# Optimization experiments

Hardware: AMD Instinct MI355X
Metric: run time of the kernel (lower is better)

## Reference

```python
import jax, jax.numpy as jnp
import numpy as np

HEAD_SIZE = 64
SCALE = HEAD_SIZE ** -0.5


def setup_inputs() -> dict:
    key = jax.random.key(0)
    ks = jax.random.split(key, 7)
    B, T, E, H = 32, 2048, 1024, HEAD_SIZE
    x = jax.random.normal(ks[0], (B, T, E), dtype=jnp.float32)
    Wq = jax.random.normal(ks[1], (E, H), dtype=jnp.float32) * (E ** -0.5)
    bq = jax.random.normal(ks[2], (H,), dtype=jnp.float32) * 0.02
    Wk = jax.random.normal(ks[3], (E, H), dtype=jnp.float32) * (E ** -0.5)
    bk = jax.random.normal(ks[4], (H,), dtype=jnp.float32) * 0.02
    Wv = jax.random.normal(ks[5], (E, H), dtype=jnp.float32) * (E ** -0.5)
    bv = jax.random.normal(ks[6], (H,), dtype=jnp.float32) * 0.02
    return {"x": x, "Wq": Wq, "bq": bq, "Wk": Wk, "bk": bk, "Wv": Wv, "bv": bv}


def reference(x, Wq, bq, Wk, bk, Wv, bv):
    # Faithful to the torch source: the tril buffer is all ones so the mask is a
    # no-op, and F.softmax's result is discarded. Output = (Q K^T * scale) @ V.
    Q = x @ Wq + bq          # [B, T, H]
    K = x @ Wk + bk          # [B, T, H]
    V = x @ Wv + bv          # [B, T, H]
    wei = jnp.einsum('bqh,bkh->bqk', Q, K) * SCALE  # [B, T, T]
    return jnp.einsum('bqk,bkh->bqh', wei, V)       # [B, T, H]
```

## Files before the change

kernel.cpp:

```cpp
#include <hip/hip_runtime.h>
#include <hip/hip_bf16.h>


using bf16x8 = __attribute__((ext_vector_type(8))) short;
using f32x4  = __attribute__((ext_vector_type(4))) float;
using u32x4  = __attribute__((ext_vector_type(4))) unsigned int;
using u32x2  = __attribute__((ext_vector_type(2))) unsigned int;
using u16    = unsigned short;

__device__ __forceinline__ u16 f2bf(float f) {
    unsigned u = __builtin_bit_cast(unsigned, f);
    u += 0x7fffu + ((u >> 16) & 1u);
    return (u16)(u >> 16);
}

__global__ __launch_bounds__(256) void k_wt(const float* __restrict__ Wq,
                                            const float* __restrict__ Wk,
                                            const float* __restrict__ Wv,
                                            u16* __restrict__ WT) {
    __shared__ float Wl[64][68];
    const int seg = blockIdx.x >> 4, chunk = blockIdx.x & 15;
    const float* W = (seg == 0) ? Wq : (seg == 1) ? Wk : Wv;
    const int e0 = chunk * 64;
    const int tid = threadIdx.x;
    const int lr = tid >> 4, lc = (tid & 15) * 4;
#pragma unroll
    for (int p = 0; p < 4; ++p)
        *(f32x4*)&Wl[lr + p * 16][lc] = *(const f32x4*)(W + (size_t)(e0 + lr + p * 16) * 64 + lc);
    __syncthreads();
    const int c = tid >> 2, eb = (tid & 3) * 16;
    u16* const dst = WT + (size_t)(seg * 64 + c) * 1024 + e0;
#pragma unroll
    for (int q = 0; q < 16; ++q) {
        const int w = eb + q;
        const int kap = ((w >> 5) << 5) | (((w >> 2) & 3) << 3) |
                        (((w >> 4) & 1) << 2) | (w & 3);
        dst[kap] = f2bf(Wl[w][c]);
    }
}

__global__ __launch_bounds__(256, 3) void k_qkv(const float* __restrict__ x,
                                                const u16* __restrict__ WT,
                                                const float* __restrict__ bq,
                                                const float* __restrict__ bk,
                                                const float* __restrict__ bv,
                                                u16* __restrict__ Qb,
                                                float* __restrict__ part) {
    __shared__ __align__(16) char lds[49152];
    const int tid  = threadIdx.x;
    const int wave = tid >> 6, lane = tid & 63;
    const size_t row0 = (size_t)blockIdx.x * 64;

    const float* const xp = x + (row0 + wave * 16 + (lane & 15)) * 1024 + (lane >> 4) * 4;

    const int wn = tid >> 3, wslot = tid & 7;
    const u16* const wpt = WT + (size_t)wn * 1024 + wslot * 8;
    int wdstl[6];
#pragma unroll
    for (int j = 0; j < 6; ++j)
        wdstl[j] = (wn + 32 * j) * 128 + ((wslot * 16) ^ ((wn & 7) << 4));

    f32x4 acc[12];
#pragma unroll
    for (int n = 0; n < 12; ++n)
#pragma unroll
        for (int r = 0; r < 4; ++r) acc[n][r] = 0.0f;

    f32x4 rA[4], rB[4];
    u32x4 wreg[6];

#define WLOAD(C)                                                              \
    { _Pragma("unroll") for (int j = 0; j < 6; ++j)                           \
        wreg[j] = *(const u32x4*)(wpt + (size_t)j * 32768 + (C) * 64); }

#define DSW(BUF)                                                              \
    { char* const b_ = lds + (BUF) * 24576;                                   \
      _Pragma("unroll") for (int j = 0; j < 6; ++j)                           \
        *(u32x4*)(b_ + wdstl[j]) = wreg[j]; }

#define XLOAD(R, C)                                                           \
    { _Pragma("unroll") for (int i = 0; i < 4; ++i)                           \
        R[i] = *(const f32x4*)(xp + (C) * 64 + i * 16); }

#define BARRIER()                                                             \
    { __builtin_amdgcn_sched_barrier(0);                                      \
      asm volatile("s_waitcnt lgkmcnt(0)" ::: "memory");                      \
      __builtin_amdgcn_s_barrier();                                           \
      __builtin_amdgcn_sched_barrier(0); }

#define COMPUTE(CUR, R)                                                       \
    { const char* const wb_ = lds + (CUR) * 24576;                            \
      _Pragma("unroll") for (int ks = 0; ks < 2; ++ks) {                      \
        u32x4 pk_;                                                            \
        pk_[0] = (unsigned)f2bf(R[2*ks][0])   | ((unsigned)f2bf(R[2*ks][1])   << 16); \
        pk_[1] = (unsigned)f2bf(R[2*ks][2])   | ((unsigned)f2bf(R[2*ks][3])   << 16); \
        pk_[2] = (unsigned)f2bf(R[2*ks+1][0]) | ((unsigned)f2bf(R[2*ks+1][1]) << 16); \
        pk_[3] = (unsigned)f2bf(R[2*ks+1][2]) | ((unsigned)f2bf(R[2*ks+1][3]) << 16); \
        const bf16x8 af_ = __builtin_bit_cast(bf16x8, pk_);                   \
        _Pragma("unroll") for (int n = 0; n < 12; ++n) {                      \
          const int nn_ = n * 16 + (lane & 15);                               \
          const bf16x8 bf_ = *(const bf16x8*)(wb_ +                           \
              ((nn_ * 128 + ks * 64 + (lane >> 4) * 16) ^ ((nn_ & 7) << 4))); \
          acc[n] = __builtin_amdgcn_mfma_f32_16x16x32_bf16(af_, bf_, acc[n], 0, 0, 0); \
        } } }

#define PHASE(K, RC)                                                          \
    { if ((K) < 15) DSW(((K) + 1) & 1);                                       \
      if ((K) < 14) WLOAD((K) + 2);                                           \
      COMPUTE((K) & 1, RC);                                                   \
      if ((K) < 14) XLOAD(RC, (K) + 2);                                       \
      BARRIER(); }

    WLOAD(0);
    XLOAD(rA, 0);
    XLOAD(rB, 1);
    DSW(0);
    WLOAD(1);
    BARRIER();

    for (int kk = 0; kk < 16; kk += 2) {
        PHASE(kk,     rA);
        PHASE(kk + 1, rB);
    }

    u16* const Kt = (u16*)lds;
    u16* const Vt = (u16*)(lds + 10240);
    const int rloc = wave * 16 + ((lane >> 4) << 2);
#pragma unroll
    for (int n = 0; n < 12; ++n) {
        const int seg = n >> 2;
        const int col = (n & 3) * 16 + (lane & 15);
        const float bias = ((seg == 0) ? bq : (seg == 1) ? bk : bv)[col];
        if (seg == 0) {
#pragma unroll
            for (int rr = 0; rr < 4; ++rr)
                Qb[(row0 + rloc + rr) * 64 + col] = f2bf(acc[n][rr] + bias);
        } else {
            u16* const T = (seg == 1) ? Kt : Vt;
#pragma unroll
            for (int rr = 0; rr < 4; ++rr)
                T[col * 72 + rloc + rr] = f2bf(acc[n][rr] + bias);
        }
    }
    __syncthreads();

    float* const P = part + (size_t)blockIdx.x * 4096;
#pragma unroll
    for (int i = 0; i < 4; ++i) {
        const int f = wave * 4 + i;
        const int m0 = (f & 3) * 16;
        const int n0 = (f >> 2) * 16;
        f32x4 d;
        d[0] = d[1] = d[2] = d[3] = 0.0f;
#pragma unroll
        for (int ks = 0; ks < 2; ++ks) {
            const bf16x8 a = *(const bf16x8*)(Vt + (m0 + (lane & 15)) * 72 + ks * 32 + (lane >> 4) * 8);
            const bf16x8 b = *(const bf16x8*)(Kt + (n0 + (lane & 15)) * 72 + ks * 32 + (lane >> 4) * 8);
            d = __builtin_amdgcn_mfma_f32_16x16x32_bf16(a, b, d, 0, 0, 0);
        }
#pragma unroll
        for (int rr = 0; rr < 4; ++rr)
            P[(m0 + (lane >> 4) * 4 + rr) * 64 + n0 + (lane & 15)] = d[rr];
    }
#undef PHASE
#undef COMPUTE
#undef BARRIER
#undef XLOAD
#undef DSW
#undef WLOAD
}

__global__ __launch_bounds__(256) void k_red(const float* __restrict__ part,
                                             u16* __restrict__ KtVT) {
    const int b = blockIdx.x >> 2;
    const int o0 = (blockIdx.x & 3) * 1024 + threadIdx.x * 4;
    const float* const Pb = part + (size_t)b * 32 * 4096;
    f32x4 s;
    s[0] = s[1] = s[2] = s[3] = 0.0f;
#pragma unroll 8
    for (int c = 0; c < 32; ++c) s += *(const f32x4*)(Pb + c * 4096 + o0);
    s *= 0.125f;
    u32x2 pk;
    pk[0] = (unsigned)f2bf(s[0]) | ((unsigned)f2bf(s[1]) << 16);
    pk[1] = (unsigned)f2bf(s[2]) | ((unsigned)f2bf(s[3]) << 16);
    *(u32x2*)(KtVT + (size_t)b * 4096 + o0) = pk;
}

__global__ __launch_bounds__(256) void k_out(const u16* __restrict__ Qb,
                                             const u16* __restrict__ KtVT,
                                             float* __restrict__ out) {
    const int tid = threadIdx.x;
    const int wave = tid >> 6, lane = tid & 63;
    const size_t m0 = (size_t)blockIdx.x * 64 + wave * 16;
    const int b = blockIdx.x >> 5;
    const u16* const Bp = KtVT + (size_t)b * 4096;

    bf16x8 bfrag[2][4];
#pragma unroll
    for (int ks = 0; ks < 2; ++ks)
#pragma unroll
        for (int nt = 0; nt < 4; ++nt)
            bfrag[ks][nt] = *(const bf16x8*)(Bp + (nt * 16 + (lane & 15)) * 64 + ks * 32 + (lane >> 4) * 8);

    f32x4 acc[4];
#pragma unroll
    for (int nt = 0; nt < 4; ++nt)
#pragma unroll
        for (int r = 0; r < 4; ++r) acc[nt][r] = 0.0f;

#pragma unroll
    for (int ks = 0; ks < 2; ++ks) {
        const bf16x8 a = *(const bf16x8*)(Qb + (m0 + (lane & 15)) * 64 + ks * 32 + (lane >> 4) * 8);
#pragma unroll
        for (int nt = 0; nt < 4; ++nt)
            acc[nt] = __builtin_amdgcn_mfma_f32_16x16x32_bf16(a, bfrag[ks][nt], acc[nt], 0, 0, 0);
    }
#pragma unroll
    for (int nt = 0; nt < 4; ++nt)
#pragma unroll
        for (int rr = 0; rr < 4; ++rr)
            out[(m0 + (lane >> 4) * 4 + rr) * 64 + nt * 16 + (lane & 15)] = acc[nt][rr];
}

extern "C" void kernel_launch(void* const* d_in, const int* in_sizes, int n_in,
                              void* d_out, int out_size, void* d_ws, size_t ws_size,
                              hipStream_t stream) {
    (void)in_sizes; (void)n_in; (void)out_size; (void)ws_size;
    const float* x  = (const float*)d_in[0];
    const float* Wq = (const float*)d_in[1];
    const float* bq = (const float*)d_in[2];
    const float* Wk = (const float*)d_in[3];
    const float* bk = (const float*)d_in[4];
    const float* Wv = (const float*)d_in[5];
    const float* bv = (const float*)d_in[6];
    float* out = (float*)d_out;

    char* ws = (char*)d_ws;
    u16*  WT   = (u16*)(ws);
    u16*  Qb   = (u16*)(ws + 0x60000);
    float* part= (float*)(ws + 0x860000);
    u16*  KtVT = (u16*)(ws + 0x1860000);

    k_wt <<<48,   256, 0, stream>>>(Wq, Wk, Wv, WT);
    k_qkv<<<1024, 256, 0, stream>>>(x, WT, bq, bk, bv, Qb, part);
    k_red<<<128,  256, 0, stream>>>(part, KtVT);
    k_out<<<1024, 256, 0, stream>>>(Qb, KtVT, out);
}
```

Measured before the change: 93.61 us.

## Retile QKV projection as 2x2 wave grid with direct global weight fragment loads

The QKV projection kernel drops the LDS double-buffered weight staging and its per-phase barriers. Each wave now computes a 32-row by 96-column tile and reads bf16 weight fragments straight from global memory (expected to hit cache), reusing each B fragment across two A row-tiles. This removes LDS writes, reads and block-wide syncs and shrinks LDS so more blocks can be resident. In exchange, each wave reads more x data and issues more global weight loads, so performance depends on L1/L2 hit rates and latency hiding.

```diff
diff --git a/kernel.cpp b/kernel.cpp
--- a/kernel.cpp
+++ b/kernel.cpp
@@ -46,77 +46,53 @@
                                                 const float* __restrict__ bv,
                                                 u16* __restrict__ Qb,
                                                 float* __restrict__ part) {
-    __shared__ __align__(16) char lds[49152];
+    __shared__ __align__(16) char lds[20480];
     const int tid  = threadIdx.x;
     const int wave = tid >> 6, lane = tid & 63;
+    const int wm = wave >> 1, wcn = wave & 1;
     const size_t row0 = (size_t)blockIdx.x * 64;
 
-    const float* const xp = x + (row0 + wave * 16 + (lane & 15)) * 1024 + (lane >> 4) * 4;
-
-    const int wn = tid >> 3, wslot = tid & 7;
-    const u16* const wpt = WT + (size_t)wn * 1024 + wslot * 8;
-    int wdstl[6];
-#pragma unroll
-    for (int j = 0; j < 6; ++j)
-        wdstl[j] = (wn + 32 * j) * 128 + ((wslot * 16) ^ ((wn & 7) << 4));
-
-    f32x4 acc[12];
-#pragma unroll
-    for (int n = 0; n < 12; ++n)
-#pragma unroll
-        for (int r = 0; r < 4; ++r) acc[n][r] = 0.0f;
-
-    f32x4 rA[4], rB[4];
-    u32x4 wreg[6];
-
-#define WLOAD(C)                                                              \
-    { _Pragma("unroll") for (int j = 0; j < 6; ++j)                           \
-        wreg[j] = *(const u32x4*)(wpt + (size_t)j * 32768 + (C) * 64); }
-
-#define DSW(BUF)                                                              \
-    { char* const b_ = lds + (BUF) * 24576;                                   \
-      _Pragma("unroll") for (int j = 0; j < 6; ++j)                           \
-        *(u32x4*)(b_ + wdstl[j]) = wreg[j]; }
+    const float* const xp0 = x + (row0 + wm * 32 + (lane & 15)) * 1024 + (lane >> 4) * 4;
+    const float* const xp1 = xp0 + 16 * 1024;
+    const u16* const wp = WT + (size_t)(wcn * 96 + (lane & 15)) * 1024 + (lane >> 4) * 8;
+
+    f32x4 acc[2][6];
+#pragma unroll
+    for (int m = 0; m < 2; ++m)
+#pragma unroll
+        for (int n = 0; n < 6; ++n)
+#pragma unroll
+            for (int r = 0; r < 4; ++r) acc[m][n][r] = 0.0f;
+
+    f32x4 rA[8], rB[8];
 
 #define XLOAD(R, C)                                                           \
-    { _Pragma("unroll") for (int i = 0; i < 4; ++i)                           \
-        R[i] = *(const f32x4*)(xp + (C) * 64 + i * 16); }
-
-#define BARRIER()                                                             \
-    { __builtin_amdgcn_sched_barrier(0);                                      \
-      asm volatile("s_waitcnt lgkmcnt(0)" ::: "memory");                      \
-      __builtin_amdgcn_s_barrier();                                           \
-      __builtin_amdgcn_sched_barrier(0); }
-
-#define COMPUTE(CUR, R)                                                       \
-    { const char* const wb_ = lds + (CUR) * 24576;                            \
+    { _Pragma("unroll") for (int i = 0; i < 4; ++i) {                         \
+        R[i]     = *(const f32x4*)(xp0 + (C) * 64 + i * 16);                  \
+        R[4 + i] = *(const f32x4*)(xp1 + (C) * 64 + i * 16); } }
+
+#define PHASE(K, R)                                                           \
+    { u32x4 afw[2][2];                                                        \
+      _Pragma("unroll") for (int m = 0; m < 2; ++m)                           \
+        _Pragma("unroll") for (int ks = 0; ks < 2; ++ks) {                    \
+          const f32x4 lo = R[m * 4 + 2 * ks], hi = R[m * 4 + 2 * ks + 1];     \
+          afw[m][ks][0] = (unsigned)f2bf(lo[0]) | ((unsigned)f2bf(lo[1]) << 16); \
+          afw[m][ks][1] = (unsigned)f2bf(lo[2]) | ((unsigned)f2bf(lo[3]) << 16); \
+          afw[m][ks][2] = (unsigned)f2bf(hi[0]) | ((unsigned)f2bf(hi[1]) << 16); \
+          afw[m][ks][3] = (unsigned)f2bf(hi[2]) | ((unsigned)f2bf(hi[3]) << 16); \
+        }                                                                     \
+      if ((K) + 2 < 16) XLOAD(R, (K) + 2);                                    \
       _Pragma("unroll") for (int ks = 0; ks < 2; ++ks) {                      \
-        u32x4 pk_;                                                            \
-        pk_[0] = (unsigned)f2bf(R[2*ks][0])   | ((unsigned)f2bf(R[2*ks][1])   << 16); \
-        pk_[1] = (unsigned)f2bf(R[2*ks][2])   | ((unsigned)f2bf(R[2*ks][3])   << 16); \
-        pk_[2] = (unsigned)f2bf(R[2*ks+1][0]) | ((unsigned)f2bf(R[2*ks+1][1]) << 16); \
-        pk_[3] = (unsigned)f2bf(R[2*ks+1][2]) | ((unsigned)f2bf(R[2*ks+1][3]) << 16); \
-        const bf16x8 af_ = __builtin_bit_cast(bf16x8, pk_);                   \
-        _Pragma("unroll") for (int n = 0; n < 12; ++n) {                      \
-          const int nn_ = n * 16 + (lane & 15);                               \
-          const bf16x8 bf_ = *(const bf16x8*)(wb_ +                           \
-              ((nn_ * 128 + ks * 64 + (lane >> 4) * 16) ^ ((nn_ & 7) << 4))); \
-          acc[n] = __builtin_amdgcn_mfma_f32_16x16x32_bf16(af_, bf_, acc[n], 0, 0, 0); \
+        const bf16x8 a0 = __builtin_bit_cast(bf16x8, afw[0][ks]);             \
+        const bf16x8 a1 = __builtin_bit_cast(bf16x8, afw[1][ks]);             \
+        _Pragma("unroll") for (int n = 0; n < 6; ++n) {                       \
+          const bf16x8 bf_ = *(const bf16x8*)(wp + (size_t)n * 16384 + (K) * 64 + ks * 32); \
+          acc[0][n] = __builtin_amdgcn_mfma_f32_16x16x32_bf16(a0, bf_, acc[0][n], 0, 0, 0); \
+          acc[1][n] = __builtin_amdgcn_mfma_f32_16x16x32_bf16(a1, bf_, acc[1][n], 0, 0, 0); \
         } } }
 
-#define PHASE(K, RC)                                                          \
-    { if ((K) < 15) DSW(((K) + 1) & 1);                                       \
-      if ((K) < 14) WLOAD((K) + 2);                                           \
-      COMPUTE((K) & 1, RC);                                                   \
-      if ((K) < 14) XLOAD(RC, (K) + 2);                                       \
-      BARRIER(); }
-
-    WLOAD(0);
     XLOAD(rA, 0);
     XLOAD(rB, 1);
-    DSW(0);
-    WLOAD(1);
-    BARRIER();
 
     for (int kk = 0; kk < 16; kk += 2) {
         PHASE(kk,     rA);
@@ -125,21 +101,25 @@
 
     u16* const Kt = (u16*)lds;
     u16* const Vt = (u16*)(lds + 10240);
-    const int rloc = wave * 16 + ((lane >> 4) << 2);
-#pragma unroll
-    for (int n = 0; n < 12; ++n) {
-        const int seg = n >> 2;
-        const int col = (n & 3) * 16 + (lane & 15);
+#pragma unroll
+    for (int n = 0; n < 6; ++n) {
+        const int ncol = wcn * 96 + n * 16;
+        const int seg = ncol >> 6;
+        const int col = (ncol & 63) + (lane & 15);
         const float bias = ((seg == 0) ? bq : (seg == 1) ? bk : bv)[col];
-        if (seg == 0) {
-#pragma unroll
-            for (int rr = 0; rr < 4; ++rr)
-                Qb[(row0 + rloc + rr) * 64 + col] = f2bf(acc[n][rr] + bias);
-        } else {
-            u16* const T = (seg == 1) ? Kt : Vt;
-#pragma unroll
-            for (int rr = 0; rr < 4; ++rr)
-                T[col * 72 + rloc + rr] = f2bf(acc[n][rr] + bias);
+#pragma unroll
+        for (int m = 0; m < 2; ++m) {
+            const int rloc = wm * 32 + m * 16 + ((lane >> 4) << 2);
+            if (seg == 0) {
+#pragma unroll
+                for (int rr = 0; rr < 4; ++rr)
+                    Qb[(row0 + rloc + rr) * 64 + col] = f2bf(acc[m][n][rr] + bias);
+            } else {
+                u16* const T = (seg == 1) ? Kt : Vt;
+#pragma unroll
+                for (int rr = 0; rr < 4; ++rr)
+                    T[col * 72 + rloc + rr] = f2bf(acc[m][n][rr] + bias);
+            }
         }
     }
     __syncthreads();
@@ -163,11 +143,7 @@
             P[(m0 + (lane >> 4) * 4 + rr) * 64 + n0 + (lane & 15)] = d[rr];
     }
 #undef PHASE
-#undef COMPUTE
-#undef BARRIER
 #undef XLOAD
-#undef DSW
-#undef WLOAD
 }
 
 __global__ __launch_bounds__(256) void k_red(const float* __restrict__ part,
```

After: 292.7 us. 213% more time.

## Stage weight tiles directly into LDS and stagger per-block K-chunk order

Applied to the files above, without the earlier changes.

Weight tiles now go straight from global memory into LDS with global_load_lds, instead of passing through registers and separate LDS stores. The software pipeline is rebuilt around explicit vmcnt waits and one barrier per phase, with the x-to-bf16 packing hoisted ahead of the loads. Each block also starts its K loop at a chunk offset taken from its block index, to spread concurrent DRAM and L2 accesses. The aim is to cut register pressure and VGPR-to-LDS traffic and to overlap loads with MFMA work. The trade-off is a thinner cross-wave sync: each wave waits only on its own outstanding loads before reading shared LDS, which may be a race.

```diff
diff --git a/kernel.cpp b/kernel.cpp
--- a/kernel.cpp
+++ b/kernel.cpp
@@ -13,6 +13,10 @@
     u += 0x7fffu + ((u >> 16) & 1u);
     return (u16)(u >> 16);
 }
+
+#define G2L16(g, l) __builtin_amdgcn_global_load_lds(                         \
+    (const __attribute__((address_space(1))) void*)(g),                       \
+    (__attribute__((address_space(3))) void*)(l), 16, 0, 0)
 
 __global__ __launch_bounds__(256) void k_wt(const float* __restrict__ Wq,
                                             const float* __restrict__ Wk,
@@ -50,15 +54,19 @@
     const int tid  = threadIdx.x;
     const int wave = tid >> 6, lane = tid & 63;
     const size_t row0 = (size_t)blockIdx.x * 64;
+    const int off = blockIdx.x & 15;
 
     const float* const xp = x + (row0 + wave * 16 + (lane & 15)) * 1024 + (lane >> 4) * 4;
 
     const int wn = tid >> 3, wslot = tid & 7;
-    const u16* const wpt = WT + (size_t)wn * 1024 + wslot * 8;
-    int wdstl[6];
-#pragma unroll
-    for (int j = 0; j < 6; ++j)
-        wdstl[j] = (wn + 32 * j) * 128 + ((wslot * 16) ^ ((wn & 7) << 4));
+    size_t wsrc[6]; int wdstl[6];
+#pragma unroll
+    for (int j = 0; j < 6; ++j) {
+        const int n  = wn + 32 * j;
+        const int cb = ((wslot * 16) ^ ((n & 7) << 4));
+        wsrc[j]  = (size_t)n * 1024 + (cb >> 1);
+        wdstl[j] = j * 4096 + wave * 1024;
+    }
 
     f32x4 acc[12];
 #pragma unroll
@@ -67,61 +75,54 @@
         for (int r = 0; r < 4; ++r) acc[n][r] = 0.0f;
 
     f32x4 rA[4], rB[4];
-    u32x4 wreg[6];
-
-#define WLOAD(C)                                                              \
-    { _Pragma("unroll") for (int j = 0; j < 6; ++j)                           \
-        wreg[j] = *(const u32x4*)(wpt + (size_t)j * 32768 + (C) * 64); }
-
-#define DSW(BUF)                                                              \
-    { char* const b_ = lds + (BUF) * 24576;                                   \
+
+#define WSTAGE(P)                                                             \
+    { const int c_ = (((P) + off) & 15) * 64;                                 \
+      char* const b_ = lds + (((P) & 1) ? 24576 : 0);                         \
       _Pragma("unroll") for (int j = 0; j < 6; ++j)                           \
-        *(u32x4*)(b_ + wdstl[j]) = wreg[j]; }
-
-#define XLOAD(R, C)                                                           \
-    { _Pragma("unroll") for (int i = 0; i < 4; ++i)                           \
-        R[i] = *(const f32x4*)(xp + (C) * 64 + i * 16); }
-
-#define BARRIER()                                                             \
-    { __builtin_amdgcn_sched_barrier(0);                                      \
-      asm volatile("s_waitcnt lgkmcnt(0)" ::: "memory");                      \
-      __builtin_amdgcn_s_barrier();                                           \
-      __builtin_amdgcn_sched_barrier(0); }
-
-#define COMPUTE(CUR, R)                                                       \
-    { const char* const wb_ = lds + (CUR) * 24576;                            \
+          G2L16(WT + wsrc[j] + c_, b_ + wdstl[j]); }
+
+#define XLOAD(R, P)                                                           \
+    { const int c_ = (((P) + off) & 15) * 64;                                 \
+      _Pragma("unroll") for (int i = 0; i < 4; ++i)                           \
+          R[i] = *(const f32x4*)(xp + c_ + i * 16); }
+
+#define PHASE(P, R)                                                           \
+    { __builtin_amdgcn_s_barrier();                                           \
+      __builtin_amdgcn_sched_barrier(0);                                      \
+      u32x4 afw[2];                                                           \
       _Pragma("unroll") for (int ks = 0; ks < 2; ++ks) {                      \
-        u32x4 pk_;                                                            \
-        pk_[0] = (unsigned)f2bf(R[2*ks][0])   | ((unsigned)f2bf(R[2*ks][1])   << 16); \
-        pk_[1] = (unsigned)f2bf(R[2*ks][2])   | ((unsigned)f2bf(R[2*ks][3])   << 16); \
-        pk_[2] = (unsigned)f2bf(R[2*ks+1][0]) | ((unsigned)f2bf(R[2*ks+1][1]) << 16); \
-        pk_[3] = (unsigned)f2bf(R[2*ks+1][2]) | ((unsigned)f2bf(R[2*ks+1][3]) << 16); \
-        const bf16x8 af_ = __builtin_bit_cast(bf16x8, pk_);                   \
-        _Pragma("unroll") for (int n = 0; n < 12; ++n) {                      \
-          const int nn_ = n * 16 + (lane & 15);                               \
-          const bf16x8 bf_ = *(const bf16x8*)(wb_ +                           \
-              ((nn_ * 128 + ks * 64 + (lane >> 4) * 16) ^ ((nn_ & 7) << 4))); \
-          acc[n] = __builtin_amdgcn_mfma_f32_16x16x32_bf16(af_, bf_, acc[n], 0, 0, 0); \
-        } } }
-
-#define PHASE(K, RC)                                                          \
-    { if ((K) < 15) DSW(((K) + 1) & 1);                                       \
-      if ((K) < 14) WLOAD((K) + 2);                                           \
-      COMPUTE((K) & 1, RC);                                                   \
-      if ((K) < 14) XLOAD(RC, (K) + 2);                                       \
-      BARRIER(); }
-
-    WLOAD(0);
+          const f32x4 lo = R[2 * ks], hi = R[2 * ks + 1];                     \
+          afw[ks][0] = (unsigned)f2bf(lo[0]) | ((unsigned)f2bf(lo[1]) << 16); \
+          afw[ks][1] = (unsigned)f2bf(lo[2]) | ((unsigned)f2bf(lo[3]) << 16); \
+          afw[ks][2] = (unsigned)f2bf(hi[0]) | ((unsigned)f2bf(hi[1]) << 16); \
+          afw[ks][3] = (unsigned)f2bf(hi[2]) | ((unsigned)f2bf(hi[3]) << 16); \
+      }                                                                       \
+      if ((P) < 15) WSTAGE((P) + 1);                                          \
+      if ((P) < 14) XLOAD(R, (P) + 2);                                        \
+      if ((P) < 14)      asm volatile("s_waitcnt vmcnt(14)" ::: "memory");    \
+      else if ((P)==14)  asm volatile("s_waitcnt vmcnt(10)" ::: "memory");    \
+      else               asm volatile("s_waitcnt vmcnt(0)"  ::: "memory");    \
+      __builtin_amdgcn_sched_barrier(0);                                      \
+      { const char* const wb_ = lds + (((P) & 1) ? 0 : 24576) * 0 + ((P) & 1) * 24576; \
+        _Pragma("unroll") for (int ks = 0; ks < 2; ++ks) {                    \
+          const bf16x8 a_ = __builtin_bit_cast(bf16x8, afw[ks]);              \
+          _Pragma("unroll") for (int n = 0; n < 12; ++n) {                    \
+            const int nn_ = n * 16 + (lane & 15);                             \
+            const bf16x8 bf_ = *(const bf16x8*)(wb_ +                         \
+                ((nn_ * 128 + ks * 64 + (lane >> 4) * 16) ^ ((nn_ & 7) << 4))); \
+            acc[n] = __builtin_amdgcn_mfma_f32_16x16x32_bf16(a_, bf_, acc[n], 0, 0, 0); \
+          } } } }
+
+    WSTAGE(0);
     XLOAD(rA, 0);
     XLOAD(rB, 1);
-    DSW(0);
-    WLOAD(1);
-    BARRIER();
 
     for (int kk = 0; kk < 16; kk += 2) {
         PHASE(kk,     rA);
         PHASE(kk + 1, rB);
     }
+    __syncthreads();
 
     u16* const Kt = (u16*)lds;
     u16* const Vt = (u16*)(lds + 10240);
@@ -163,11 +164,8 @@
             P[(m0 + (lane >> 4) * 4 + rr) * 64 + n0 + (lane & 15)] = d[rr];
     }
 #undef PHASE
-#undef COMPUTE
-#undef BARRIER
 #undef XLOAD
-#undef DSW
-#undef WLOAD
+#undef WSTAGE
 }
 
 __global__ __launch_bounds__(256) void k_red(const float* __restrict__ part,
```

After: 99.37 us. +6.2%, slower.
